# Optimization experiments

Measured on AMD Instinct MI355X. Metric: run time of the kernel, lower is better.

The kernel has to match this reference:

```python
import jax, jax.numpy as jnp
import numpy as np


def setup_inputs() -> dict:
    key = jax.random.key(0)
    k1, k2, k3, k4 = jax.random.split(key, 4)
    b, c_in, t, h, w = 8, 64, 16, 64, 64
    c_out, kh, kw = 64, 3, 3
    x = jax.random.normal(k1, (b, c_in, t, h, w), dtype=jnp.float32)
    alpha = jax.random.uniform(k2, (b, c_in, t, 1, 1), dtype=jnp.float32)
    fan_in = c_in * kh * kw
    weight = jax.random.normal(k3, (c_out, c_in, kh, kw), dtype=jnp.float32) / np.sqrt(fan_in)
    bias = jax.random.normal(k4, (c_out,), dtype=jnp.float32) * 0.05
    return {"x": x, "alpha": alpha, "weight": weight, "bias": bias}


def reference(x, alpha, weight, bias):
    # x: (b, c_in, t, h, w); alpha: (b, c_in, t, 1, 1)
    # weight: (c_out, c_in, kh, kw); bias: (c_out,)
    b, c_in, t, h, w = x.shape
    c_out, _, kh, kw = weight.shape
    pad = ((kh // 2, kh // 2), (kw // 2, kw // 2))  # padding=1 for 3x3
    # per-(b,t) calibrated weights: alpha scales the c_in dim (cal_dim='cin')
    a = jnp.transpose(alpha[..., 0, 0], (0, 2, 1))          # (b, t, c_in)
    w_bt = a[:, :, None, :, None, None] * weight[None, None]  # (b, t, c_out, c_in, kh, kw)
    xs = jnp.transpose(x, (0, 2, 1, 3, 4)).reshape(b * t, 1, c_in, h, w)
    ws = w_bt.reshape(b * t, c_out, c_in, kh, kw)

    def conv_one(xi, wi):
        return jax.lax.conv_general_dilated(
            xi, wi, window_strides=(1, 1), padding=pad,
            dimension_numbers=("NCHW", "OIHW", "NCHW"))[0]

    out = jax.vmap(conv_one)(xs, ws)                          # (b*t, c_out, h, w)
    out = out + bias[None, :, None, None]
    out = out.reshape(b, t, c_out, h, w).transpose(0, 2, 1, 3, 4)
    return out  # (b, c_out, t, h, w)
```

## Files before the change

### kernel.cpp

```cpp
#include <hip/hip_runtime.h>


#define CIN  64
#define COUT 64
#define TT   16
#define BB   8
#define HH   64
#define WW   64
#define NSTEP 8

typedef __attribute__((ext_vector_type(8))) short bf16x8;
typedef __attribute__((ext_vector_type(4))) float f32x4;

__device__ __forceinline__ unsigned short f2bf(float f) {
    union { float f; unsigned u; } v; v.f = f;
    unsigned r = (v.u + 0x7FFF + ((v.u >> 16) & 1)) >> 16;
    return (unsigned short)r;
}

__global__ __launch_bounds__(256) void prep_w(const float* __restrict__ wgt,
                                              unsigned short* __restrict__ wb) {
    int idx = blockIdx.x * 256 + threadIdx.x;
    if (idx < COUT * CIN * 9) {
        int co  = idx / (CIN * 9);
        int r   = idx - co * (CIN * 9);
        int ci  = r / 9;
        int tap = r - ci * 9;
        int q    = co >> 4;
        int co_l = co & 15;
        int kc   = ci >> 5;
        int kg   = (ci >> 3) & 3;
        int e    = ci & 7;
        wb[(((((q * 9 + tap) * 2 + kc) * 4 + kg) * 16) + co_l) * 8 + e] = f2bf(wgt[idx]);
    }
}

__global__ __launch_bounds__(256, 2) void conv6(const float* __restrict__ x,
                                                const float* __restrict__ alpha,
                                                const short* __restrict__ wb,
                                                const float* __restrict__ bias,
                                                float* __restrict__ out) {
    __shared__ __align__(16) short xs[8 * 4224];

    const int orig = blockIdx.x;
    const int blk  = (orig & 7) * 64 + (orig >> 3);
    const int qy   = blk & 3;
    const int bt   = blk >> 2;
    const int t    = bt & 15;
    const int b    = bt >> 4;
    const int yb   = qy * 16;
    const int tid  = threadIdx.x;
    const int wv   = tid >> 6;
    const int lane = tid & 63;
    const int co_l = lane & 15;
    const int kg   = lane >> 4;
    const int mg   = wv >> 1;
    const int rw   = wv & 1;

    bf16x8 wreg[2][9][2];
#pragma unroll
    for (int m = 0; m < 2; ++m)
#pragma unroll
        for (int tap = 0; tap < 9; ++tap)
#pragma unroll
            for (int kc = 0; kc < 2; ++kc)
                wreg[m][tap][kc] = *(const bf16x8*)(
                    wb + ((((mg * 2 + m) * 9 + tap) * 2 + kc) * 64 + lane) * 8);

    float av[2][8];
#pragma unroll
    for (int gi = 0; gi < 2; ++gi)
#pragma unroll
        for (int j = 0; j < 8; ++j) {
            float a = alpha[(b * CIN + (wv + gi * 4) * 8 + j) * TT + t];
            av[gi][j] = __builtin_bit_cast(
                float, __builtin_amdgcn_readfirstlane(__builtin_bit_cast(int, a)));
        }

    const float* xbase0 = x + (size_t)((b * CIN + wv * 8) * TT + t) * (HH * WW);
    const float* xbase1 = x + (size_t)((b * CIN + (wv + 4) * 8) * TT + t) * (HH * WW);

    if (tid < 128) {
        int slot = tid >> 4, col = (tid >> 3) & 1, sg = tid & 7;
        int4 z = {0, 0, 0, 0};
        *(int4*)(xs + slot * 4224 + col * 4160 + sg * 8) = z;
    }

    float fb[2][2][8];
    auto stage_load = [&](int gy0) {
#pragma unroll
        for (int r = 0; r < 2; ++r) {
            const int gy = gy0 + r;
            const bool ok = (unsigned)gy < HH;
            const float* p0 = xbase0 + gy * WW + lane;
            const float* p1 = xbase1 + gy * WW + lane;
#pragma unroll
            for (int j = 0; j < 8; ++j) {
                fb[r][0][j] = ok ? p0[j * 65536] : 0.0f;
                fb[r][1][j] = ok ? p1[j * 65536] : 0.0f;
            }
        }
    };
    auto stage_store = [&](int s0) {
#pragma unroll
        for (int r = 0; r < 2; ++r)
#pragma unroll
            for (int gi = 0; gi < 2; ++gi) {
                const int g = wv + gi * 4;
                int4 o;
                o.x = (int)f2bf(fb[r][gi][0] * av[gi][0]) | ((int)f2bf(fb[r][gi][1] * av[gi][1]) << 16);
                o.y = (int)f2bf(fb[r][gi][2] * av[gi][2]) | ((int)f2bf(fb[r][gi][3] * av[gi][3]) << 16);
                o.z = (int)f2bf(fb[r][gi][4] * av[gi][4]) | ((int)f2bf(fb[r][gi][5] * av[gi][5]) << 16);
                o.w = (int)f2bf(fb[r][gi][6] * av[gi][6]) | ((int)f2bf(fb[r][gi][7] * av[gi][7]) << 16);
                *(int4*)(xs + ((s0 + r) & 7) * 4224 + (lane + 1) * 64 + ((g ^ (lane & 7)) * 8)) = o;
            }
    };

    stage_load(yb - 1); stage_store(0);
    stage_load(yb + 1); stage_store(2);

    int si[3][2];
#pragma unroll
    for (int dxi = 0; dxi < 3; ++dxi)
#pragma unroll
        for (int kc = 0; kc < 2; ++kc) {
            int wx = co_l + dxi - 1;
            si[dxi][kc] = (wx + 1) * 64 + (((kc * 4 + kg) ^ (wx & 7)) * 8);
        }

    __syncthreads();

    for (int it = 0; it < NSTEP; ++it) {
        if (it < NSTEP - 1) stage_load(yb + 2 * it + 3);

        f32x4 acc[2][4] = {};
        __builtin_amdgcn_s_setprio(1);
#pragma unroll
        for (int tap = 0; tap < 9; ++tap) {
            const int ky  = tap / 3;
            const int dxi = tap - 3 * ky;
            const short* rowp = xs + ((2 * it + rw + ky) & 7) * 4224;
#pragma unroll
            for (int kc = 0; kc < 2; ++kc) {
                const short* bp = rowp + si[dxi][kc];
#pragma unroll
                for (int n = 0; n < 4; ++n) {
                    bf16x8 bfr = *(const bf16x8*)(bp + n * 1024);
                    acc[0][n] = __builtin_amdgcn_mfma_f32_16x16x32_bf16(
                        wreg[0][tap][kc], bfr, acc[0][n], 0, 0, 0);
                    acc[1][n] = __builtin_amdgcn_mfma_f32_16x16x32_bf16(
                        wreg[1][tap][kc], bfr, acc[1][n], 0, 0, 0);
                }
            }
        }
        __builtin_amdgcn_s_setprio(0);

        const int y = yb + 2 * it + rw;
#pragma unroll
        for (int m = 0; m < 2; ++m)
#pragma unroll
            for (int rr = 0; rr < 4; ++rr) {
                const int co = (mg * 2 + m) * 16 + kg * 4 + rr;
                const float bv = bias[co];
                float* op = out + (size_t)(((b * COUT + co) * TT + t) * HH + y) * WW;
#pragma unroll
                for (int n = 0; n < 4; ++n)
                    op[n * 16 + co_l] = acc[m][n][rr] + bv;
            }

        if (it < NSTEP - 1) stage_store(2 * it + 4);
        __syncthreads();
    }
}

extern "C" void kernel_launch(void* const* d_in, const int* in_sizes, int n_in,
                              void* d_out, int out_size, void* d_ws, size_t ws_size,
                              hipStream_t stream) {
    const float* x      = (const float*)d_in[0];
    const float* alpha  = (const float*)d_in[1];
    const float* weight = (const float*)d_in[2];
    const float* bias   = (const float*)d_in[3];
    float* out          = (float*)d_out;

    unsigned short* wb = (unsigned short*)d_ws;

    hipLaunchKernelGGL(prep_w, dim3(144), dim3(256), 0, stream, weight, wb);
    hipLaunchKernelGGL(conv6, dim3(8 * 64), dim3(256), 0, stream,
                       x, alpha, (const short*)wb, bias, out);
}
```

Baseline: 269.1 us.

## Split conv block across 512 threads with 6-slot LDS ring buffer

Doubles the workgroup to 8 waves so each wave computes half the output columns and loads one channel group instead of two. The LDS row ring shrinks from 8 to 6 slots, and the store of the next rows plus the barrier move before the output writes, so the global stores overlap with the next iteration. It also drops s_setprio and fully unrolls the main loop. The aim is more waves in flight to hide global-load and store latency, at the cost of each wave holding the full weight register set, which limits occupancy under the new launch bounds.

New measurement: 485.0 us. +80.3%, slower.

```diff
diff --git a/kernel.cpp b/kernel.cpp
--- a/kernel.cpp
+++ b/kernel.cpp
@@ -35,12 +35,12 @@
     }
 }
 
-__global__ __launch_bounds__(256, 2) void conv6(const float* __restrict__ x,
+__global__ __launch_bounds__(512, 4) void conv7(const float* __restrict__ x,
                                                 const float* __restrict__ alpha,
                                                 const short* __restrict__ wb,
                                                 const float* __restrict__ bias,
                                                 float* __restrict__ out) {
-    __shared__ __align__(16) short xs[8 * 4224];
+    __shared__ __align__(16) short xs[6 * 4224];
 
     const int orig = blockIdx.x;
     const int blk  = (orig & 7) * 64 + (orig >> 3);
@@ -54,8 +54,9 @@
     const int lane = tid & 63;
     const int co_l = lane & 15;
     const int kg   = lane >> 4;
-    const int mg   = wv >> 1;
     const int rw   = wv & 1;
+    const int mg   = (wv >> 1) & 1;
+    const int ns   = wv >> 2;
 
     bf16x8 wreg[2][9][2];
 #pragma unroll
@@ -67,93 +68,93 @@
                 wreg[m][tap][kc] = *(const bf16x8*)(
                     wb + ((((mg * 2 + m) * 9 + tap) * 2 + kc) * 64 + lane) * 8);
 
-    float av[2][8];
+    float av[8];
 #pragma unroll
-    for (int gi = 0; gi < 2; ++gi)
-#pragma unroll
-        for (int j = 0; j < 8; ++j) {
-            float a = alpha[(b * CIN + (wv + gi * 4) * 8 + j) * TT + t];
-            av[gi][j] = __builtin_bit_cast(
-                float, __builtin_amdgcn_readfirstlane(__builtin_bit_cast(int, a)));
-        }
+    for (int j = 0; j < 8; ++j) {
+        float a = alpha[(b * CIN + wv * 8 + j) * TT + t];
+        av[j] = __builtin_bit_cast(
+            float, __builtin_amdgcn_readfirstlane(__builtin_bit_cast(int, a)));
+    }
 
-    const float* xbase0 = x + (size_t)((b * CIN + wv * 8) * TT + t) * (HH * WW);
-    const float* xbase1 = x + (size_t)((b * CIN + (wv + 4) * 8) * TT + t) * (HH * WW);
+    const float* xb = x + (size_t)((b * CIN + wv * 8) * TT + t) * (HH * WW);
 
-    if (tid < 128) {
+    if (tid < 96) {
         int slot = tid >> 4, col = (tid >> 3) & 1, sg = tid & 7;
         int4 z = {0, 0, 0, 0};
         *(int4*)(xs + slot * 4224 + col * 4160 + sg * 8) = z;
     }
 
-    float fb[2][2][8];
-    auto stage_load = [&](int gy0) {
+    auto stage_load = [&](int gy, float* f) {
+        const bool ok = (unsigned)gy < HH;
+        const float* p = xb + gy * WW + lane;
 #pragma unroll
-        for (int r = 0; r < 2; ++r) {
-            const int gy = gy0 + r;
-            const bool ok = (unsigned)gy < HH;
-            const float* p0 = xbase0 + gy * WW + lane;
-            const float* p1 = xbase1 + gy * WW + lane;
-#pragma unroll
-            for (int j = 0; j < 8; ++j) {
-                fb[r][0][j] = ok ? p0[j * 65536] : 0.0f;
-                fb[r][1][j] = ok ? p1[j * 65536] : 0.0f;
-            }
-        }
+        for (int j = 0; j < 8; ++j) f[j] = ok ? p[j * 65536] : 0.0f;
     };
-    auto stage_store = [&](int s0) {
-#pragma unroll
-        for (int r = 0; r < 2; ++r)
-#pragma unroll
-            for (int gi = 0; gi < 2; ++gi) {
-                const int g = wv + gi * 4;
-                int4 o;
-                o.x = (int)f2bf(fb[r][gi][0] * av[gi][0]) | ((int)f2bf(fb[r][gi][1] * av[gi][1]) << 16);
-                o.y = (int)f2bf(fb[r][gi][2] * av[gi][2]) | ((int)f2bf(fb[r][gi][3] * av[gi][3]) << 16);
-                o.z = (int)f2bf(fb[r][gi][4] * av[gi][4]) | ((int)f2bf(fb[r][gi][5] * av[gi][5]) << 16);
-                o.w = (int)f2bf(fb[r][gi][6] * av[gi][6]) | ((int)f2bf(fb[r][gi][7] * av[gi][7]) << 16);
-                *(int4*)(xs + ((s0 + r) & 7) * 4224 + (lane + 1) * 64 + ((g ^ (lane & 7)) * 8)) = o;
-            }
+    auto stage_store = [&](int slot, const float* f) {
+        int4 o;
+        o.x = (int)f2bf(f[0] * av[0]) | ((int)f2bf(f[1] * av[1]) << 16);
+        o.y = (int)f2bf(f[2] * av[2]) | ((int)f2bf(f[3] * av[3]) << 16);
+        o.z = (int)f2bf(f[4] * av[4]) | ((int)f2bf(f[5] * av[5]) << 16);
+        o.w = (int)f2bf(f[6] * av[6]) | ((int)f2bf(f[7] * av[7]) << 16);
+        *(int4*)(xs + slot * 4224 + (lane + 1) * 64 + ((wv ^ (lane & 7)) * 8)) = o;
     };
 
-    stage_load(yb - 1); stage_store(0);
-    stage_load(yb + 1); stage_store(2);
+    {
+        float fp[4][8];
+#pragma unroll
+        for (int r = 0; r < 4; ++r) stage_load(yb - 1 + r, fp[r]);
+#pragma unroll
+        for (int r = 0; r < 4; ++r) stage_store(r, fp[r]);
+    }
 
     int si[3][2];
 #pragma unroll
     for (int dxi = 0; dxi < 3; ++dxi)
 #pragma unroll
         for (int kc = 0; kc < 2; ++kc) {
-            int wx = co_l + dxi - 1;
+            int wx = ns * 32 + co_l + dxi - 1;
             si[dxi][kc] = (wx + 1) * 64 + (((kc * 4 + kg) ^ (wx & 7)) * 8);
         }
 
     __syncthreads();
 
+    float fb[2][8];
+#pragma unroll
     for (int it = 0; it < NSTEP; ++it) {
-        if (it < NSTEP - 1) stage_load(yb + 2 * it + 3);
+        const int s0 = (2 * it) % 6;
 
-        f32x4 acc[2][4] = {};
-        __builtin_amdgcn_s_setprio(1);
+        if (it < NSTEP - 1) {
+            stage_load(yb + 2 * it + 3, fb[0]);
+            stage_load(yb + 2 * it + 4, fb[1]);
+        }
+
+        f32x4 acc[2][2] = {};
 #pragma unroll
         for (int tap = 0; tap < 9; ++tap) {
             const int ky  = tap / 3;
             const int dxi = tap - 3 * ky;
-            const short* rowp = xs + ((2 * it + rw + ky) & 7) * 4224;
+            int u = s0 + rw + ky; if (u >= 6) u -= 6;
+            const short* rowp = xs + u * 4224;
 #pragma unroll
             for (int kc = 0; kc < 2; ++kc) {
                 const short* bp = rowp + si[dxi][kc];
 #pragma unroll
-                for (int n = 0; n < 4; ++n) {
-                    bf16x8 bfr = *(const bf16x8*)(bp + n * 1024);
-                    acc[0][n] = __builtin_amdgcn_mfma_f32_16x16x32_bf16(
-                        wreg[0][tap][kc], bfr, acc[0][n], 0, 0, 0);
-                    acc[1][n] = __builtin_amdgcn_mfma_f32_16x16x32_bf16(
-                        wreg[1][tap][kc], bfr, acc[1][n], 0, 0, 0);
+                for (int nl = 0; nl < 2; ++nl) {
+                    bf16x8 bfr = *(const bf16x8*)(bp + nl * 1024);
+                    acc[0][nl] = __builtin_amdgcn_mfma_f32_16x16x32_bf16(
+                        wreg[0][tap][kc], bfr, acc[0][nl], 0, 0, 0);
+                    acc[1][nl] = __builtin_amdgcn_mfma_f32_16x16x32_bf16(
+                        wreg[1][tap][kc], bfr, acc[1][nl], 0, 0, 0);
                 }
             }
         }
-        __builtin_amdgcn_s_setprio(0);
+
+        if (it < NSTEP - 1) {
+            stage_store((2 * it + 4) % 6, fb[0]);
+            stage_store((2 * it + 5) % 6, fb[1]);
+        }
+
+        if (it < NSTEP - 1) __syncthreads();
 
         const int y = yb + 2 * it + rw;
 #pragma unroll
@@ -164,12 +165,9 @@
                 const float bv = bias[co];
                 float* op = out + (size_t)(((b * COUT + co) * TT + t) * HH + y) * WW;
 #pragma unroll
-                for (int n = 0; n < 4; ++n)
-                    op[n * 16 + co_l] = acc[m][n][rr] + bv;
+                for (int nl = 0; nl < 2; ++nl)
+                    op[ns * 32 + nl * 16 + co_l] = acc[m][nl][rr] + bv;
             }
-
-        if (it < NSTEP - 1) stage_store(2 * it + 4);
-        __syncthreads();
     }
 }
 
@@ -185,6 +183,6 @@
     unsigned short* wb = (unsigned short*)d_ws;
 
     hipLaunchKernelGGL(prep_w, dim3(144), dim3(256), 0, stream, weight, wb);
-    hipLaunchKernelGGL(conv6, dim3(8 * 64), dim3(256), 0, stream,
+    hipLaunchKernelGGL(conv7, dim3(8 * 64), dim3(512), 0, stream,
                        x, alpha, (const short*)wb, bias, out);
 }
```

## Use float2 row loads, 6-slot LDS ring, and move store/sync before epilogue

Applied to the files above, without the earlier changes.

Switches the global x staging to float2 loads with each half-wave fetching one of the two rows, which halves the load instruction count. The LDS ring shrinks from 8 to 6 row slots. The LDS store and barrier now run before the output writes, so the global stores can overlap the next iteration, and the output writes become nontemporal. It also drops the s_setprio hints and fully unrolls the iteration loop, which may raise code size and register pressure.

Result: slower. 293.0 us (+8.9%).

```diff
diff --git a/kernel.cpp b/kernel.cpp
--- a/kernel.cpp
+++ b/kernel.cpp
@@ -35,12 +35,12 @@
     }
 }
 
-__global__ __launch_bounds__(256, 2) void conv6(const float* __restrict__ x,
+__global__ __launch_bounds__(256, 2) void conv8(const float* __restrict__ x,
                                                 const float* __restrict__ alpha,
                                                 const short* __restrict__ wb,
                                                 const float* __restrict__ bias,
                                                 float* __restrict__ out) {
-    __shared__ __align__(16) short xs[8 * 4224];
+    __shared__ __align__(16) short xs[6 * 4224];
 
     const int orig = blockIdx.x;
     const int blk  = (orig & 7) * 64 + (orig >> 3);
@@ -56,6 +56,8 @@
     const int kg   = lane >> 4;
     const int mg   = wv >> 1;
     const int rw   = wv & 1;
+    const int rh   = lane >> 5;
+    const int pp   = (lane & 31) * 2;
 
     bf16x8 wreg[2][9][2];
 #pragma unroll
@@ -77,47 +79,49 @@
                 float, __builtin_amdgcn_readfirstlane(__builtin_bit_cast(int, a)));
         }
 
-    const float* xbase0 = x + (size_t)((b * CIN + wv * 8) * TT + t) * (HH * WW);
-    const float* xbase1 = x + (size_t)((b * CIN + (wv + 4) * 8) * TT + t) * (HH * WW);
+    const float* xb0 = x + (size_t)((b * CIN + wv * 8) * TT + t) * (HH * WW);
+    const float* xb1 = x + (size_t)((b * CIN + (wv + 4) * 8) * TT + t) * (HH * WW);
 
-    if (tid < 128) {
+    if (tid < 96) {
         int slot = tid >> 4, col = (tid >> 3) & 1, sg = tid & 7;
         int4 z = {0, 0, 0, 0};
         *(int4*)(xs + slot * 4224 + col * 4160 + sg * 8) = z;
     }
 
-    float fb[2][2][8];
+    float2 fb[2][8];
     auto stage_load = [&](int gy0) {
+        const int gy = gy0 + rh;
+        const bool ok = (unsigned)gy < HH;
+        const float2* p0 = (const float2*)(xb0 + (size_t)gy0 * WW) + lane;
+        const float2* p1 = (const float2*)(xb1 + (size_t)gy0 * WW) + lane;
+        const float2 z = {0.0f, 0.0f};
 #pragma unroll
-        for (int r = 0; r < 2; ++r) {
-            const int gy = gy0 + r;
-            const bool ok = (unsigned)gy < HH;
-            const float* p0 = xbase0 + gy * WW + lane;
-            const float* p1 = xbase1 + gy * WW + lane;
-#pragma unroll
-            for (int j = 0; j < 8; ++j) {
-                fb[r][0][j] = ok ? p0[j * 65536] : 0.0f;
-                fb[r][1][j] = ok ? p1[j * 65536] : 0.0f;
-            }
+        for (int j = 0; j < 8; ++j) {
+            fb[0][j] = ok ? p0[j * 32768] : z;
+            fb[1][j] = ok ? p1[j * 32768] : z;
         }
     };
-    auto stage_store = [&](int s0) {
+    auto stage_store = [&](int sA, int sB) {
+        const int sl = rh ? sB : sA;
 #pragma unroll
-        for (int r = 0; r < 2; ++r)
-#pragma unroll
-            for (int gi = 0; gi < 2; ++gi) {
-                const int g = wv + gi * 4;
-                int4 o;
-                o.x = (int)f2bf(fb[r][gi][0] * av[gi][0]) | ((int)f2bf(fb[r][gi][1] * av[gi][1]) << 16);
-                o.y = (int)f2bf(fb[r][gi][2] * av[gi][2]) | ((int)f2bf(fb[r][gi][3] * av[gi][3]) << 16);
-                o.z = (int)f2bf(fb[r][gi][4] * av[gi][4]) | ((int)f2bf(fb[r][gi][5] * av[gi][5]) << 16);
-                o.w = (int)f2bf(fb[r][gi][6] * av[gi][6]) | ((int)f2bf(fb[r][gi][7] * av[gi][7]) << 16);
-                *(int4*)(xs + ((s0 + r) & 7) * 4224 + (lane + 1) * 64 + ((g ^ (lane & 7)) * 8)) = o;
-            }
+        for (int gi = 0; gi < 2; ++gi) {
+            const int g = wv + gi * 4;
+            int4 e, o;
+            e.x = (int)f2bf(fb[gi][0].x * av[gi][0]) | ((int)f2bf(fb[gi][1].x * av[gi][1]) << 16);
+            e.y = (int)f2bf(fb[gi][2].x * av[gi][2]) | ((int)f2bf(fb[gi][3].x * av[gi][3]) << 16);
+            e.z = (int)f2bf(fb[gi][4].x * av[gi][4]) | ((int)f2bf(fb[gi][5].x * av[gi][5]) << 16);
+            e.w = (int)f2bf(fb[gi][6].x * av[gi][6]) | ((int)f2bf(fb[gi][7].x * av[gi][7]) << 16);
+            o.x = (int)f2bf(fb[gi][0].y * av[gi][0]) | ((int)f2bf(fb[gi][1].y * av[gi][1]) << 16);
+            o.y = (int)f2bf(fb[gi][2].y * av[gi][2]) | ((int)f2bf(fb[gi][3].y * av[gi][3]) << 16);
+            o.z = (int)f2bf(fb[gi][4].y * av[gi][4]) | ((int)f2bf(fb[gi][5].y * av[gi][5]) << 16);
+            o.w = (int)f2bf(fb[gi][6].y * av[gi][6]) | ((int)f2bf(fb[gi][7].y * av[gi][7]) << 16);
+            *(int4*)(xs + sl * 4224 + (pp + 1) * 64 + ((g ^ (pp & 7)) * 8))       = e;
+            *(int4*)(xs + sl * 4224 + (pp + 2) * 64 + ((g ^ ((pp + 1) & 7)) * 8)) = o;
+        }
     };
 
-    stage_load(yb - 1); stage_store(0);
-    stage_load(yb + 1); stage_store(2);
+    stage_load(yb - 1); stage_store(0, 1);
+    stage_load(yb + 1); stage_store(2, 3);
 
     int si[3][2];
 #pragma unroll
@@ -130,16 +134,19 @@
 
     __syncthreads();
 
+#pragma unroll
     for (int it = 0; it < NSTEP; ++it) {
+        const int s0 = (2 * it) % 6;
+
         if (it < NSTEP - 1) stage_load(yb + 2 * it + 3);
 
         f32x4 acc[2][4] = {};
-        __builtin_amdgcn_s_setprio(1);
 #pragma unroll
         for (int tap = 0; tap < 9; ++tap) {
             const int ky  = tap / 3;
             const int dxi = tap - 3 * ky;
-            const short* rowp = xs + ((2 * it + rw + ky) & 7) * 4224;
+            int u = s0 + rw + ky; if (u >= 6) u -= 6;
+            const short* rowp = xs + u * 4224;
 #pragma unroll
             for (int kc = 0; kc < 2; ++kc) {
                 const short* bp = rowp + si[dxi][kc];
@@ -153,7 +160,10 @@
                 }
             }
         }
-        __builtin_amdgcn_s_setprio(0);
+
+        if (it < NSTEP - 1) stage_store((2 * it + 4) % 6, (2 * it + 5) % 6);
+
+        if (it < NSTEP - 1) __syncthreads();
 
         const int y = yb + 2 * it + rw;
 #pragma unroll
@@ -165,11 +175,8 @@
                 float* op = out + (size_t)(((b * COUT + co) * TT + t) * HH + y) * WW;
 #pragma unroll
                 for (int n = 0; n < 4; ++n)
-                    op[n * 16 + co_l] = acc[m][n][rr] + bv;
+                    __builtin_nontemporal_store(acc[m][n][rr] + bv, &op[n * 16 + co_l]);
             }
-
-        if (it < NSTEP - 1) stage_store(2 * it + 4);
-        __syncthreads();
     }
 }
 
@@ -185,6 +192,6 @@
     unsigned short* wb = (unsigned short*)d_ws;
 
     hipLaunchKernelGGL(prep_w, dim3(144), dim3(256), 0, stream, weight, wb);
-    hipLaunchKernelGGL(conv6, dim3(8 * 64), dim3(256), 0, stream,
+    hipLaunchKernelGGL(conv8, dim3(8 * 64), dim3(256), 0, stream,
                        x, alpha, (const short*)wb, bias, out);
 }
```
